# Performance work log

Measured on AMD Instinct MI355X. Metric: run time of the kernel, lower is better.

## Reference

```python
import jax, jax.numpy as jnp
import numpy as np

# e3nn normalize2mom gain for tanh (1/sqrt(E[tanh(z)^2]), z~N(0,1))
TANH_GAIN = 1.5927116870880127
B, M_IN, M_HID, M_OUT = 8192, 64, 128, 64

_W_SPECS = {
    'b1_l1_w0': (64, 64), 'b1_l1_w1': (64, 64), 'b1_l2_w0': (64, 64), 'b1_l2_w1': (64, 64),
    'b1_tp_ss': (64, 64, 128), 'b1_tp_vv': (64, 64, 128), 'b1_tp_sv': (64, 64, 128), 'b1_tp_vs': (64, 64, 128),
    'b1_g_ws': (128, 128), 'b1_g_wg': (128, 128), 'b1_g_wv': (128, 128),
    'b1_o_w0': (128, 128), 'b1_o_w1': (128, 128),
    'b2_l1_w0': (128, 128), 'b2_l1_w1': (128, 128), 'b2_l2_w0': (128, 128), 'b2_l2_w1': (128, 128),
    'b2_tp_ss': (128, 128, 128), 'b2_tp_vv': (128, 128, 128), 'b2_tp_sv': (128, 128, 128), 'b2_tp_vs': (128, 128, 128),
    'b2_g_ws': (128, 128), 'b2_g_wg': (128, 128), 'b2_g_wv': (128, 128),
    'b2_o_w0': (128, 128), 'b2_o_w1': (128, 128),
    'f_w0': (128, 64), 'f_w1': (128, 64),
}


def setup_inputs() -> dict:
    key = jax.random.key(0)
    ks = jax.random.split(key, len(_W_SPECS) + 1)
    d = {'x': jax.random.normal(ks[0], (B, M_IN + 3 * M_IN), jnp.float32)}
    for i, (name, shp) in enumerate(_W_SPECS.items()):
        d[name] = jax.random.normal(ks[i + 1], shp, jnp.float32)  # e3nn weights ~ N(0,1)
    return d


def _lin(s, v, w0, w1):
    # o3.Linear on 'Mx0e+Mx1o': per-irrep block matmul, path_normalization='element' -> 1/sqrt(fan_in)
    c = 1.0 / np.sqrt(w0.shape[0])
    return (s @ w0) * c, jnp.einsum('bui,uw->bwi', v, w1) * c


def _tp(s1, v1, s2, v2, wss, wvv, wsv, wvs):
    # FullyConnectedTensorProduct, irrep_normalization='component', path_normalization='element'.
    # Two uvw paths feed each output irrep -> path_weight = sqrt(dim_out / (2*M*M)).
    # CG values: w3j(0,0,0)=1; w3j(0,1,1)=delta/sqrt(3); w3j(1,0,1)=delta/sqrt(3); w3j(1,1,0)=delta/sqrt(3).
    M = s1.shape[-1]
    c = 1.0 / (M * np.sqrt(2.0))
    s = c * jnp.einsum('bu,bv,uvw->bw', s1, s2, wss) \
        + (c / np.sqrt(3.0)) * jnp.einsum('bui,bvi,uvw->bw', v1, v2, wvv)
    v = c * (jnp.einsum('bu,bvi,uvw->bwi', s1, v2, wsv)
             + jnp.einsum('bui,bv,uvw->bwi', v1, s2, wvs))
    return s, v


def _gate(s, v, ws, wg, wv):
    # LearnableGate: o3.Linear to (scalars | gate scalars | vectors), then e3nn Gate
    # (tanh w/ normalize2mom gain on scalars and gates; elementwise gate*vector has unit path weight).
    c = 1.0 / np.sqrt(ws.shape[0])
    sl = (s @ ws) * c
    g = (s @ wg) * c
    vl = jnp.einsum('bui,uw->bwi', v, wv) * c
    return TANH_GAIN * jnp.tanh(sl), (TANH_GAIN * jnp.tanh(g))[..., None] * vl


def _block(s, v, p):
    l1w0, l1w1, l2w0, l2w1, wss, wvv, wsv, wvs, gws, gwg, gwv, ow0, ow1 = p
    s1, v1 = _lin(s, v, l1w0, l1w1)
    s2, v2 = _lin(s, v, l2w0, l2w1)
    s, v = _tp(s1, v1, s2, v2, wss, wvv, wsv, wvs)
    s, v = _gate(s, v, gws, gwg, gwv)
    return _lin(s, v, ow0, ow1)


def _forward(x, *w):
    s = x[:, :M_IN]
    v = x[:, M_IN:].reshape(x.shape[0], M_IN, 3)
    s, v = _block(s, v, w[0:13])
    s, v = _block(s, v, w[13:26])
    s, v = _lin(s, v, w[26], w[27])
    return jnp.concatenate([s, v.reshape(v.shape[0], -1)], axis=-1)


def reference(x, b1_l1_w0, b1_l1_w1, b1_l2_w0, b1_l2_w1, b1_tp_ss, b1_tp_vv, b1_tp_sv, b1_tp_vs, b1_g_ws, b1_g_wg, b1_g_wv, b1_o_w0, b1_o_w1, b2_l1_w0, b2_l1_w1, b2_l2_w0, b2_l2_w1, b2_tp_ss, b2_tp_vv, b2_tp_sv, b2_tp_vs, b2_g_ws, b2_g_wg, b2_g_wv, b2_o_w0, b2_o_w1, f_w0, f_w1):
    return _forward(x, b1_l1_w0, b1_l1_w1, b1_l2_w0, b1_l2_w1, b1_tp_ss, b1_tp_vv, b1_tp_sv, b1_tp_vs, b1_g_ws, b1_g_wg, b1_g_wv, b1_o_w0, b1_o_w1, b2_l1_w0, b2_l1_w1, b2_l2_w0, b2_l2_w1, b2_tp_ss, b2_tp_vv, b2_tp_sv, b2_tp_vs, b2_g_ws, b2_g_wg, b2_g_wv, b2_o_w0, b2_o_w1, f_w0, f_w1)
```

## Files before the change

kernel.cpp:

```cpp
#include <hip/hip_runtime.h>
#include <math.h>

typedef _Float16 f16;
typedef __attribute__((ext_vector_type(8))) _Float16 half8;
typedef __attribute__((ext_vector_type(4))) _Float16 half4;
typedef __attribute__((ext_vector_type(4))) float floatx4;

#define NB 8192

struct ConvJob { const float* src; f16* dst; int K; int N; int ucount; float scale; int swz; };
struct ConvJobs { ConvJob j[28]; };

__global__ void convert_w(ConvJobs JJ) {
    ConvJob jb = JJ.j[blockIdx.z];
    int u = blockIdx.x;
    if (u >= jb.ucount) return;
    __shared__ f16 tile[128 * 136];
    const int K = jb.K, N = jb.N;
    const int npad = N + 8;
    const int nsh = (N == 128) ? 7 : 6;
    const int ksh = (K == 128) ? 7 : 6;
    const float* src = jb.src + (size_t)u * K * N;
    for (int idx = threadIdx.x; idx < K * N; idx += 256) {
        int k = idx >> nsh, n = idx & (N - 1);
        tile[k * npad + n] = (f16)(src[idx] * jb.scale);
    }
    __syncthreads();
    f16* dst = jb.dst + (size_t)u * N * K;
    for (int idx = threadIdx.x; idx < N * K; idx += 256) {
        int n = idx >> ksh, rem = idx & (K - 1);
        int g2 = rem >> 3, jj = rem & 7;
        int g = jb.swz ? (g2 ^ (n & jb.swz)) : g2;
        int k = g * 8 + jj;
        dst[idx] = tile[k * npad + n];
    }
}

__global__ void x_to_planes(const float* __restrict__ x, f16* s_p, f16* v0, f16* v1, f16* v2) {
    int t = blockIdx.x * 256 + threadIdx.x;
    if (t >= NB * 64) return;
    int b = t >> 6, u = t & 63;
    const float* xr = x + (size_t)b * 256;
    s_p[t] = (f16)xr[u];
    v0[t] = (f16)xr[64 + 3 * u + 0];
    v1[t] = (f16)xr[64 + 3 * u + 1];
    v2[t] = (f16)xr[64 + 3 * u + 2];
}

struct TpJob { const f16* p; const f16* q; const f16* w; float* out; int pstride; int qstride; };
struct TpJobs { TpJob j[10]; };

template <int M>
__launch_bounds__(256, (M == 128) ? 3 : 4)
__global__ void tp_unit(TpJobs JJ) {
    TpJob jb = JJ.j[blockIdx.z];
    constexpr int KC = M / 32;
    constexpr int GM = M / 8 - 1;
    constexpr int SLABH = 64 * M;
    constexpr int PIECES = SLABH / 8;
    constexpr int IPW = PIECES / 256;
    constexpr int SLABFULL = 128 * M;
    __shared__ f16 w_lds[2][SLABH];
    const int tid = threadIdx.x, lane = tid & 63, wave = tid >> 6;
    const int wm = wave & 1, wn = wave >> 1;
    const int l15 = lane & 15, quad = lane >> 4;
    const int rowBase = blockIdx.x * 128;
    const int colBase = blockIdx.y * 64;

    {
        int id = blockIdx.x + (int)gridDim.x * (blockIdx.y + (int)gridDim.y * blockIdx.z);
        int ph = (id >> 8) % 3;
        for (int i = 0; i < ph; i++) __builtin_amdgcn_s_sleep(18);
    }

    half8 qf[4][KC];
    int prow[4];
    #pragma unroll
    for (int t = 0; t < 4; t++) {
        int row = rowBase + wm * 64 + t * 16 + l15;
        prow[t] = row;
        const f16* qr = jb.q + (size_t)row * jb.qstride;
        #pragma unroll
        for (int c = 0; c < KC; c++) qf[t][c] = *(const half8*)(qr + c * 32 + quad * 8);
    }
    floatx4 acc[4][2];
    #pragma unroll
    for (int a = 0; a < 4; a++)
        #pragma unroll
        for (int b = 0; b < 2; b++) acc[a][b] = (floatx4){0.f, 0.f, 0.f, 0.f};

    int rd_off[2][KC];
    #pragma unroll
    for (int nt = 0; nt < 2; nt++) {
        int nl = wn * 32 + nt * 16 + l15;
        #pragma unroll
        for (int c = 0; c < KC; c++) {
            int g = c * 4 + quad;
            rd_off[nt][c] = nl * M + ((g ^ (nl & GM)) << 3);
        }
    }

    const int wpBase = wave * (PIECES / 4);
    const f16* wsrc0 = jb.w + (size_t)colBase * M + (size_t)(wpBase + lane) * 8;
    auto stage = [&](int u, int buf) {
        const f16* src = wsrc0 + (size_t)u * SLABFULL;
        f16* dst = &w_lds[buf][0] + (size_t)wpBase * 8;
        #pragma unroll
        for (int i = 0; i < IPW; i++) {
            __builtin_amdgcn_global_load_lds(
                (const __attribute__((address_space(1))) void*)(src + i * 64 * 8),
                (__attribute__((address_space(3))) void*)(dst + i * 64 * 8),
                16, 0, 0);
        }
    };

    stage(0, 0);
    __syncthreads();

    for (int uc = 0; uc < M / 8; uc++) {
        half8 pcur[4];
        #pragma unroll
        for (int t = 0; t < 4; t++)
            pcur[t] = *(const half8*)(jb.p + (size_t)prow[t] * jb.pstride + uc * 8);
        #pragma unroll
        for (int j = 0; j < 8; j++) {
            const int u = uc * 8 + j;
            const int cur = j & 1;
            if (j != 7 || uc != M / 8 - 1) stage(u + 1, cur ^ 1);
            #pragma unroll
            for (int c = 0; c < KC; c++) {
                half8 af[4];
                #pragma unroll
                for (int t = 0; t < 4; t++) {
                    f16 pv = pcur[t][j];
                    half8 p8 = {pv, pv, pv, pv, pv, pv, pv, pv};
                    af[t] = qf[t][c] * p8;
                }
                __builtin_amdgcn_s_setprio(1);
                #pragma unroll
                for (int nt = 0; nt < 2; nt++) {
                    half8 bf = *(const half8*)&w_lds[cur][rd_off[nt][c]];
                    #pragma unroll
                    for (int t = 0; t < 4; t++)
                        acc[t][nt] = __builtin_amdgcn_mfma_f32_16x16x32_f16(af[t], bf, acc[t][nt], 0, 0, 0);
                }
                __builtin_amdgcn_s_setprio(0);
            }
            __syncthreads();
        }
    }
    #pragma unroll
    for (int t = 0; t < 4; t++)
        #pragma unroll
        for (int nt = 0; nt < 2; nt++) {
            int col = colBase + wn * 32 + nt * 16 + l15;
            float* orow = jb.out + (size_t)(rowBase + wm * 64 + t * 16 + quad * 4) * 128 + col;
            #pragma unroll
            for (int r = 0; r < 4; r++) orow[(size_t)r * 128] = acc[t][nt][r];
        }
}

struct SmallJob { const f16* A; const f16* W; char* out; int astride; int ostride;
                  int ocol; int cstride; int mode; int Njob; int ny;
                  const f16* Amul; int mstride;
                  const float* red0; const float* red1; const float* red2; const float* red3;
                  int nred; };
struct SmallJobs { SmallJob j[4]; };

template <int K>
__launch_bounds__(256, 2)
__global__ void small_gemm(SmallJobs JJ) {
    SmallJob jb = JJ.j[blockIdx.z];
    if ((int)blockIdx.y >= jb.ny) return;
    constexpr int KC = K / 32;
    constexpr int NP = K + 8;
    constexpr int PR = K / 8;
    constexpr int PPT = 128 * K / 8 / 256;
    __shared__ f16 w_lds[128 * NP];
    const int tid = threadIdx.x, lane = tid & 63, wave = tid >> 6;
    const int wm = wave & 1, wn = wave >> 1;
    const int l15 = lane & 15, quad = lane >> 4;
    const int rowBase = blockIdx.x * 64;
    const int nBase = blockIdx.y * 128;

    #pragma unroll
    for (int t = 0; t < PPT; t++) {
        int idx = t * 256 + tid;
        int r = idx / PR, pc = idx % PR;
        int4 v = {0, 0, 0, 0};
        if (nBase + r < jb.Njob)
            v = *(const int4*)(jb.W + (size_t)(nBase + r) * K + pc * 8);
        *(int4*)&w_lds[r * NP + pc * 8] = v;
    }
    half8 qf[2][KC];
    for (int t = 0; t < 2; t++) {
        int row = rowBase + wm * 32 + t * 16 + l15;
        if (jb.nred) {
            #pragma unroll
            for (int c = 0; c < KC; c++) {
                size_t boff = (size_t)row * 128 + c * 32 + quad * 8;
                floatx4 s0 = *(const floatx4*)(jb.red0 + boff);
                floatx4 s1 = *(const floatx4*)(jb.red0 + boff + 4);
                if (jb.nred > 1) { s0 += *(const floatx4*)(jb.red1 + boff); s1 += *(const floatx4*)(jb.red1 + boff + 4); }
                if (jb.nred > 2) { s0 += *(const floatx4*)(jb.red2 + boff); s1 += *(const floatx4*)(jb.red2 + boff + 4); }
                if (jb.nred > 3) { s0 += *(const floatx4*)(jb.red3 + boff); s1 += *(const floatx4*)(jb.red3 + boff + 4); }
                qf[t][c] = (half8){(f16)s0.x, (f16)s0.y, (f16)s0.z, (f16)s0.w,
                                   (f16)s1.x, (f16)s1.y, (f16)s1.z, (f16)s1.w};
            }
        } else {
            const f16* ar = jb.A + (size_t)row * jb.astride;
            #pragma unroll
            for (int c = 0; c < KC; c++) qf[t][c] = *(const half8*)(ar + c * 32 + quad * 8);
        }
        if (jb.Amul) {
            const f16* mr = jb.Amul + (size_t)row * jb.mstride;
            #pragma unroll
            for (int c = 0; c < KC; c++) qf[t][c] = qf[t][c] * *(const half8*)(mr + c * 32 + quad * 8);
        }
    }
    floatx4 acc[2][4];
    #pragma unroll
    for (int a = 0; a < 2; a++)
        #pragma unroll
        for (int b = 0; b < 4; b++) acc[a][b] = (floatx4){0.f, 0.f, 0.f, 0.f};
    __syncthreads();
    #pragma unroll
    for (int c = 0; c < KC; c++)
        #pragma unroll
        for (int nt = 0; nt < 4; nt++) {
            half8 bf = *(const half8*)&w_lds[(wn * 64 + nt * 16 + l15) * NP + c * 32 + quad * 8];
            #pragma unroll
            for (int t = 0; t < 2; t++)
                acc[t][nt] = __builtin_amdgcn_mfma_f32_16x16x32_f16(qf[t][c], bf, acc[t][nt], 0, 0, 0);
        }
    const float GAIN = 1.5927116870880127f;
    #pragma unroll
    for (int t = 0; t < 2; t++)
        #pragma unroll
        for (int nt = 0; nt < 4; nt++) {
            int col = nBase + wn * 64 + nt * 16 + l15;
            if (col >= jb.Njob) continue;
            int rowB = rowBase + wm * 32 + t * 16 + quad * 4;
            #pragma unroll
            for (int r = 0; r < 4; r++) {
                float v = acc[t][nt][r];
                size_t ro = (size_t)(rowB + r) * jb.ostride;
                if (jb.mode == 0)      ((f16*)jb.out)[ro + jb.ocol + col] = (f16)v;
                else if (jb.mode == 1) ((f16*)jb.out)[ro + jb.ocol + col] = (f16)(GAIN * tanhf(v));
                else                   ((float*)jb.out)[ro + jb.ocol + (size_t)col * jb.cstride] = v;
            }
        }
}

extern "C" void kernel_launch(void* const* d_in, const int* in_sizes, int n_in,
                              void* d_out, int out_size, void* d_ws, size_t ws_size,
                              hipStream_t stream) {
    const float* x = (const float*)d_in[0];
    const float* W_IN[28];
    for (int i = 0; i < 28; i++) W_IN[i] = (const float*)d_in[1 + i];

    char* base = (char*)d_ws;
    size_t off = 0;
    auto alloc = [&](size_t bytes) -> char* {
        char* p = base + off;
        off += (bytes + 255) & ~(size_t)255;
        return p;
    };
    const size_t S128 = (size_t)NB * 128;

    f16* Wl12_b1_s = (f16*)alloc(8192 * 2);
    f16* Wl12_b1_v = (f16*)alloc(8192 * 2);
    f16* Wl12_b2_s = (f16*)alloc(32768 * 2);
    f16* Wl12_b2_v = (f16*)alloc(32768 * 2);
    f16* Wtp_b1[4]; for (int i = 0; i < 4; i++) Wtp_b1[i] = (f16*)alloc((size_t)64 * 128 * 64 * 2);
    f16* Wtp_b2[4]; for (int i = 0; i < 4; i++) Wtp_b2[i] = (f16*)alloc((size_t)128 * 128 * 128 * 2);
    f16* Wg_b1_sg = (f16*)alloc(32768 * 2);
    f16* Wg_b1_v  = (f16*)alloc(16384 * 2);
    f16* Wg_b2_sg = (f16*)alloc(32768 * 2);
    f16* Wg_b2_v  = (f16*)alloc(16384 * 2);
    f16* Wo_b1_s = (f16*)alloc(16384 * 2);
    f16* Wo_b1_v = (f16*)alloc(16384 * 2);
    f16* Wo_b2_s = (f16*)alloc(16384 * 2);
    f16* Wo_b2_v = (f16*)alloc(16384 * 2);
    f16* Wf_s = (f16*)alloc(8192 * 2);
    f16* Wf_v = (f16*)alloc(8192 * 2);
    f16* s_p = (f16*)alloc((size_t)NB * 64 * 2);
    f16* v_p[3]; for (int i = 0; i < 3; i++) v_p[i] = (f16*)alloc((size_t)NB * 64 * 2);
    f16* Breg = (f16*)alloc((size_t)4 * NB * 256 * 2);
    float* Part = (float*)alloc((size_t)10 * S128 * 4);
    f16* Ereg = (f16*)alloc((size_t)5 * S128 * 2);
    f16* Freg = (f16*)alloc((size_t)4 * S128 * 2);
    (void)ws_size; (void)in_sizes; (void)n_in; (void)out_size;

    const float c_l1 = 0.125f;
    const float c128 = 0.088388347648318447f;
    const float c1 = 1.0f / (64.0f * 1.4142135623730951f);
    const float c2 = 1.0f / (128.0f * 1.4142135623730951f);
    const float i3 = 0.57735026918962584f;

    ConvJobs CJ;
    int jn = 0;
    auto CV = [&](const float* s, f16* d, int K, int N, int uc, float sc, int swz) {
        CJ.j[jn++] = ConvJob{s, d, K, N, uc, sc, swz};
    };
    CV(W_IN[0], Wl12_b1_s, 64, 64, 1, c_l1, 0);  CV(W_IN[2], Wl12_b1_s + 4096, 64, 64, 1, c_l1, 0);
    CV(W_IN[1], Wl12_b1_v, 64, 64, 1, c_l1, 0);  CV(W_IN[3], Wl12_b1_v + 4096, 64, 64, 1, c_l1, 0);
    CV(W_IN[13], Wl12_b2_s, 128, 128, 1, c128, 0); CV(W_IN[15], Wl12_b2_s + 16384, 128, 128, 1, c128, 0);
    CV(W_IN[14], Wl12_b2_v, 128, 128, 1, c128, 0); CV(W_IN[16], Wl12_b2_v + 16384, 128, 128, 1, c128, 0);
    CV(W_IN[4], Wtp_b1[0], 64, 128, 64, c1, 7);  CV(W_IN[5], Wtp_b1[1], 64, 128, 64, c1 * i3, 7);
    CV(W_IN[6], Wtp_b1[2], 64, 128, 64, c1, 7);  CV(W_IN[7], Wtp_b1[3], 64, 128, 64, c1, 7);
    CV(W_IN[17], Wtp_b2[0], 128, 128, 128, c2, 15); CV(W_IN[18], Wtp_b2[1], 128, 128, 128, c2 * i3, 15);
    CV(W_IN[19], Wtp_b2[2], 128, 128, 128, c2, 15); CV(W_IN[20], Wtp_b2[3], 128, 128, 128, c2, 15);
    CV(W_IN[8], Wg_b1_sg, 128, 128, 1, c128, 0);  CV(W_IN[9], Wg_b1_sg + 16384, 128, 128, 1, c128, 0);
    CV(W_IN[10], Wg_b1_v, 128, 128, 1, c128, 0);
    CV(W_IN[21], Wg_b2_sg, 128, 128, 1, c128, 0); CV(W_IN[22], Wg_b2_sg + 16384, 128, 128, 1, c128, 0);
    CV(W_IN[23], Wg_b2_v, 128, 128, 1, c128, 0);
    CV(W_IN[11], Wo_b1_s, 128, 128, 1, c128, 0);  CV(W_IN[12], Wo_b1_v, 128, 128, 1, c128, 0);
    CV(W_IN[24], Wo_b2_s, 128, 128, 1, c128, 0);  CV(W_IN[25], Wo_b2_v, 128, 128, 1, c128, 0);
    CV(W_IN[26], Wf_s, 128, 64, 1, c128, 0);      CV(W_IN[27], Wf_v, 128, 64, 1, c128, 0);
    convert_w<<<dim3(128, 1, 28), 256, 0, stream>>>(CJ);

    x_to_planes<<<NB * 64 / 256, 256, 0, stream>>>(x, s_p, v_p[0], v_p[1], v_p[2]);

    auto SJ = [](const f16* A, const f16* W, void* out, int as, int os, int oc, int cs,
                 int mode, int Nj, int ny, const f16* Amul, int ms) {
        return SmallJob{A, W, (char*)out, as, os, oc, cs, mode, Nj, ny, Amul, ms,
                        nullptr, nullptr, nullptr, nullptr, 0};
    };

    f16* s12 = Breg;
    f16* v12[3]; for (int i = 0; i < 3; i++) v12[i] = Breg + (size_t)(1 + i) * NB * 128;
    f16* sg_gg = Ereg;
    f16* vl[3]; for (int i = 0; i < 3; i++) vl[i] = Ereg + 2 * S128 + i * S128;
    f16* s_o = Freg; f16* v_o[3]; for (int i = 0; i < 3; i++) v_o[i] = Freg + (1 + i) * S128;

    {
        SmallJobs J;
        J.j[0] = SJ(s_p, Wl12_b1_s, s12, 64, 128, 0, 1, 0, 128, 1, nullptr, 0);
        for (int i = 0; i < 3; i++) J.j[1 + i] = SJ(v_p[i], Wl12_b1_v, v12[i], 64, 128, 0, 1, 0, 128, 1, nullptr, 0);
        small_gemm<64><<<dim3(128, 1, 4), 256, 0, stream>>>(J);
    }
    {
        TpJobs J;
        J.j[0] = TpJob{s12, s12 + 64, Wtp_b1[0], Part + 0 * S128, 128, 128};
        for (int i = 0; i < 3; i++) J.j[1 + i] = TpJob{v12[i], v12[i] + 64, Wtp_b1[1], Part + (1 + i) * S128, 128, 128};
        for (int i = 0; i < 3; i++) J.j[4 + i] = TpJob{s12, v12[i] + 64, Wtp_b1[2], Part + (4 + i) * S128, 128, 128};
        for (int i = 0; i < 3; i++) J.j[7 + i] = TpJob{v12[i], s12 + 64, Wtp_b1[3], Part + (7 + i) * S128, 128, 128};
        tp_unit<64><<<dim3(64, 2, 10), 256, 0, stream>>>(J);
    }
    {
        SmallJobs J;
        J.j[0] = SmallJob{nullptr, Wg_b1_sg, (char*)sg_gg, 128, 256, 0, 1, 1, 256, 2, nullptr, 0,
                          Part + 0 * S128, Part + 1 * S128, Part + 2 * S128, Part + 3 * S128, 4};
        for (int i = 0; i < 3; i++)
            J.j[1 + i] = SmallJob{nullptr, Wg_b1_v, (char*)vl[i], 128, 128, 0, 1, 0, 128, 1, nullptr, 0,
                                  Part + (4 + i) * S128, Part + (7 + i) * S128, nullptr, nullptr, 2};
        small_gemm<128><<<dim3(128, 2, 4), 256, 0, stream>>>(J);
    }
    {
        SmallJobs J;
        J.j[0] = SJ(sg_gg, Wo_b1_s, s_o, 256, 128, 0, 1, 0, 128, 1, nullptr, 0);
        for (int i = 0; i < 3; i++) J.j[1 + i] = SJ(vl[i], Wo_b1_v, v_o[i], 128, 128, 0, 1, 0, 128, 1, sg_gg + 128, 256);
        small_gemm<128><<<dim3(128, 1, 4), 256, 0, stream>>>(J);
    }
    f16* s12b = Breg;
    f16* v12b[3]; for (int i = 0; i < 3; i++) v12b[i] = Breg + (size_t)(1 + i) * NB * 256;
    {
        SmallJobs J;
        J.j[0] = SJ(s_o, Wl12_b2_s, s12b, 128, 256, 0, 1, 0, 256, 2, nullptr, 0);
        for (int i = 0; i < 3; i++) J.j[1 + i] = SJ(v_o[i], Wl12_b2_v, v12b[i], 128, 256, 0, 1, 0, 256, 2, nullptr, 0);
        small_gemm<128><<<dim3(128, 2, 4), 256, 0, stream>>>(J);
    }
    {
        TpJobs J;
        J.j[0] = TpJob{s12b, s12b + 128, Wtp_b2[0], Part + 0 * S128, 256, 256};
        for (int i = 0; i < 3; i++) J.j[1 + i] = TpJob{v12b[i], v12b[i] + 128, Wtp_b2[1], Part + (1 + i) * S128, 256, 256};
        for (int i = 0; i < 3; i++) J.j[4 + i] = TpJob{s12b, v12b[i] + 128, Wtp_b2[2], Part + (4 + i) * S128, 256, 256};
        for (int i = 0; i < 3; i++) J.j[7 + i] = TpJob{v12b[i], s12b + 128, Wtp_b2[3], Part + (7 + i) * S128, 256, 256};
        tp_unit<128><<<dim3(64, 2, 10), 256, 0, stream>>>(J);
    }
    {
        SmallJobs J;
        J.j[0] = SmallJob{nullptr, Wg_b2_sg, (char*)sg_gg, 128, 256, 0, 1, 1, 256, 2, nullptr, 0,
                          Part + 0 * S128, Part + 1 * S128, Part + 2 * S128, Part + 3 * S128, 4};
        for (int i = 0; i < 3; i++)
            J.j[1 + i] = SmallJob{nullptr, Wg_b2_v, (char*)vl[i], 128, 128, 0, 1, 0, 128, 1, nullptr, 0,
                                  Part + (4 + i) * S128, Part + (7 + i) * S128, nullptr, nullptr, 2};
        small_gemm<128><<<dim3(128, 2, 4), 256, 0, stream>>>(J);
    }
    {
        SmallJobs J;
        J.j[0] = SJ(sg_gg, Wo_b2_s, s_o, 256, 128, 0, 1, 0, 128, 1, nullptr, 0);
        for (int i = 0; i < 3; i++) J.j[1 + i] = SJ(vl[i], Wo_b2_v, v_o[i], 128, 128, 0, 1, 0, 128, 1, sg_gg + 128, 256);
        small_gemm<128><<<dim3(128, 1, 4), 256, 0, stream>>>(J);
    }
    {
        SmallJobs J;
        J.j[0] = SJ(s_o, Wf_s, d_out, 128, 256, 0, 1, 2, 64, 1, nullptr, 0);
        for (int i = 0; i < 3; i++) J.j[1 + i] = SJ(v_o[i], Wf_v, d_out, 128, 256, 64 + i, 3, 2, 64, 1, nullptr, 0);
        small_gemm<128><<<dim3(128, 1, 4), 256, 0, stream>>>(J);
    }
}
```

Measured before the change: 630.3 us.

## Compose consecutive linear weight matrices to eliminate two per-batch GEMM launches

Adds a compose_w kernel that multiplies the block output linear weights with the following linear weights (block1 out with block2 in, block2 out with the final linear) once per call. The batch path then applies the composed weights directly to the gate outputs, removing two small_gemm launches and the intermediate s_o/v_o buffers. The cost is a small extra weight-preparation kernel and a slightly different fp16 rounding of the composed weights, which could affect accuracy.

After: 618.2 us. About the same (-1.9%).

```diff
diff --git a/kernel.cpp b/kernel.cpp
--- a/kernel.cpp
+++ b/kernel.cpp
@@ -34,6 +34,23 @@
         int k = g * 8 + jj;
         dst[idx] = tile[k * npad + n];
     }
+}
+
+struct CompJob { const f16* wo; const f16* wl; f16* out; int N; };
+struct CompJobs { CompJob j[4]; };
+
+__global__ void compose_w(CompJobs JJ) {
+    CompJob jb = JJ.j[blockIdx.z];
+    int n = blockIdx.x;
+    if (n >= jb.N) return;
+    int k = threadIdx.x;
+    const f16* wo = jb.wo + k;
+    const f16* wl = jb.wl + (size_t)n * 128;
+    float acc = 0.f;
+    #pragma unroll 8
+    for (int m = 0; m < 128; m++)
+        acc += (float)wl[m] * (float)wo[(size_t)m * 128];
+    jb.out[(size_t)n * 128 + k] = (f16)acc;
 }
 
 __global__ void x_to_planes(const float* __restrict__ x, f16* s_p, f16* v0, f16* v1, f16* v2) {
@@ -284,12 +301,15 @@
     f16* Wo_b2_v = (f16*)alloc(16384 * 2);
     f16* Wf_s = (f16*)alloc(8192 * 2);
     f16* Wf_v = (f16*)alloc(8192 * 2);
+    f16* Wc_s_b12 = (f16*)alloc((size_t)256 * 128 * 2);
+    f16* Wc_v_b12 = (f16*)alloc((size_t)256 * 128 * 2);
+    f16* Wc_s_fin = (f16*)alloc((size_t)64 * 128 * 2);
+    f16* Wc_v_fin = (f16*)alloc((size_t)64 * 128 * 2);
     f16* s_p = (f16*)alloc((size_t)NB * 64 * 2);
     f16* v_p[3]; for (int i = 0; i < 3; i++) v_p[i] = (f16*)alloc((size_t)NB * 64 * 2);
     f16* Breg = (f16*)alloc((size_t)4 * NB * 256 * 2);
     float* Part = (float*)alloc((size_t)10 * S128 * 4);
     f16* Ereg = (f16*)alloc((size_t)5 * S128 * 2);
-    f16* Freg = (f16*)alloc((size_t)4 * S128 * 2);
     (void)ws_size; (void)in_sizes; (void)n_in; (void)out_size;
 
     const float c_l1 = 0.125f;
@@ -320,6 +340,15 @@
     CV(W_IN[26], Wf_s, 128, 64, 1, c128, 0);      CV(W_IN[27], Wf_v, 128, 64, 1, c128, 0);
     convert_w<<<dim3(128, 1, 28), 256, 0, stream>>>(CJ);
 
+    {
+        CompJobs CJ2;
+        CJ2.j[0] = CompJob{Wo_b1_s, Wl12_b2_s, Wc_s_b12, 256};
+        CJ2.j[1] = CompJob{Wo_b1_v, Wl12_b2_v, Wc_v_b12, 256};
+        CJ2.j[2] = CompJob{Wo_b2_s, Wf_s, Wc_s_fin, 64};
+        CJ2.j[3] = CompJob{Wo_b2_v, Wf_v, Wc_v_fin, 64};
+        compose_w<<<dim3(256, 1, 4), 128, 0, stream>>>(CJ2);
+    }
+
     x_to_planes<<<NB * 64 / 256, 256, 0, stream>>>(x, s_p, v_p[0], v_p[1], v_p[2]);
 
     auto SJ = [](const f16* A, const f16* W, void* out, int as, int os, int oc, int cs,
@@ -332,7 +361,6 @@
     f16* v12[3]; for (int i = 0; i < 3; i++) v12[i] = Breg + (size_t)(1 + i) * NB * 128;
     f16* sg_gg = Ereg;
     f16* vl[3]; for (int i = 0; i < 3; i++) vl[i] = Ereg + 2 * S128 + i * S128;
-    f16* s_o = Freg; f16* v_o[3]; for (int i = 0; i < 3; i++) v_o[i] = Freg + (1 + i) * S128;
 
     {
         SmallJobs J;
@@ -357,18 +385,13 @@
                                   Part + (4 + i) * S128, Part + (7 + i) * S128, nullptr, nullptr, 2};
         small_gemm<128><<<dim3(128, 2, 4), 256, 0, stream>>>(J);
     }
-    {
-        SmallJobs J;
-        J.j[0] = SJ(sg_gg, Wo_b1_s, s_o, 256, 128, 0, 1, 0, 128, 1, nullptr, 0);
-        for (int i = 0; i < 3; i++) J.j[1 + i] = SJ(vl[i], Wo_b1_v, v_o[i], 128, 128, 0, 1, 0, 128, 1, sg_gg + 128, 256);
-        small_gemm<128><<<dim3(128, 1, 4), 256, 0, stream>>>(J);
-    }
     f16* s12b = Breg;
     f16* v12b[3]; for (int i = 0; i < 3; i++) v12b[i] = Breg + (size_t)(1 + i) * NB * 256;
     {
         SmallJobs J;
-        J.j[0] = SJ(s_o, Wl12_b2_s, s12b, 128, 256, 0, 1, 0, 256, 2, nullptr, 0);
-        for (int i = 0; i < 3; i++) J.j[1 + i] = SJ(v_o[i], Wl12_b2_v, v12b[i], 128, 256, 0, 1, 0, 256, 2, nullptr, 0);
+        J.j[0] = SJ(sg_gg, Wc_s_b12, s12b, 256, 256, 0, 1, 0, 256, 2, nullptr, 0);
+        for (int i = 0; i < 3; i++)
+            J.j[1 + i] = SJ(vl[i], Wc_v_b12, v12b[i], 128, 256, 0, 1, 0, 256, 2, sg_gg + 128, 256);
         small_gemm<128><<<dim3(128, 2, 4), 256, 0, stream>>>(J);
     }
     {
@@ -390,14 +413,9 @@
     }
     {
         SmallJobs J;
-        J.j[0] = SJ(sg_gg, Wo_b2_s, s_o, 256, 128, 0, 1, 0, 128, 1, nullptr, 0);
-        for (int i = 0; i < 3; i++) J.j[1 + i] = SJ(vl[i], Wo_b2_v, v_o[i], 128, 128, 0, 1, 0, 128, 1, sg_gg + 128, 256);
+        J.j[0] = SJ(sg_gg, Wc_s_fin, d_out, 256, 256, 0, 1, 2, 64, 1, nullptr, 0);
+        for (int i = 0; i < 3; i++)
+            J.j[1 + i] = SJ(vl[i], Wc_v_fin, d_out, 128, 256, 64 + i, 3, 2, 64, 1, sg_gg + 128, 256);
         small_gemm<128><<<dim3(128, 1, 4), 256, 0, stream>>>(J);
     }
-    {
-        SmallJobs J;
-        J.j[0] = SJ(s_o, Wf_s, d_out, 128, 256, 0, 1, 2, 64, 1, nullptr, 0);
-        for (int i = 0; i < 3; i++) J.j[1 + i] = SJ(v_o[i], Wf_v, d_out, 128, 256, 64 + i, 3, 2, 64, 1, nullptr, 0);
-        small_gemm<128><<<dim3(128, 1, 4), 256, 0, stream>>>(J);
-    }
-}
+}
```
